# Performance work log

Hardware: AMD Instinct MI355X
Metric: run time of the kernel (lower is better)

The kernel has to match this reference:

```python
import jax, jax.numpy as jnp
import numpy as np

B, N, C, H = 2, 4096, 256, 4
EPS = 1e-12  # torch F.normalize eps


def setup_inputs() -> dict:
    key = jax.random.key(0)
    k1, k2, k3, k4 = jax.random.split(key, 4)
    x = jax.random.normal(k1, (B, N, C), dtype=jnp.float32)
    w_qkv = jax.random.normal(k2, (3 * C, C), dtype=jnp.float32) * (1.0 / np.sqrt(C))
    w_out = jax.random.normal(k3, (C, C), dtype=jnp.float32) * (1.0 / np.sqrt(C))
    b_out = jnp.zeros((C,), dtype=jnp.float32)
    temperature = jnp.ones((H, 1, 1), dtype=jnp.float32)
    return {"x": x, "w_qkv": w_qkv, "w_out": w_out, "b_out": b_out,
            "temperature": temperature}


def _l2norm(t):
    # torch.nn.functional.normalize(t, dim=-1): t / max(||t||_2, eps)
    n = jnp.sqrt(jnp.sum(t * t, axis=-1, keepdims=True))
    return t / jnp.maximum(n, EPS)


def reference(x, w_qkv, w_out, b_out, temperature):
    b, n, c = x.shape
    d = c // H
    qkv = x @ w_qkv.T                                   # [B,N,3C]
    qkv = qkv.reshape(b, n, 3, H, d).transpose(2, 0, 3, 1, 4)  # [3,B,H,N,d]
    q, k, v = qkv[0], qkv[1], qkv[2]                    # each [B,H,N,d]
    # transpose(-2,-1) -> [B,H,d,N]; normalize along N (per channel over tokens)
    q = _l2norm(jnp.swapaxes(q, -2, -1))                # [B,H,d,N]
    k = _l2norm(jnp.swapaxes(k, -2, -1))                # [B,H,d,N]
    v = jnp.swapaxes(v, -2, -1)                         # [B,H,d,N]
    # attn[n,m] = sum_d q[d,n] * k[d,m], scaled by learned per-head temperature
    attn = jnp.einsum('bhdn,bhdm->bhnm', q, k) * temperature  # [B,H,N,N]
    attn = jax.nn.softmax(attn, axis=-1)
    # (attn @ v^T): [B,H,N,N] @ [B,H,N,d] -> [B,H,N,d]
    out = jnp.einsum('bhnm,bhdm->bhnd', attn, v)        # [B,H,N,d]
    # faithful to source: permute(0,3,1,2) -> [B,d,H,N], then reshape(B,N,C)
    out = out.transpose(0, 3, 1, 2).reshape(b, n, c)
    return out @ w_out.T + b_out
```

## Files before the change

### kernel.cpp

```cpp
#include <hip/hip_runtime.h>

typedef _Float16 f16;
typedef f16 f16x8 __attribute__((ext_vector_type(8)));
typedef f16 f16x4 __attribute__((ext_vector_type(4)));
typedef __fp16 fp16x2 __attribute__((ext_vector_type(2)));
typedef float f32x4 __attribute__((ext_vector_type(4)));
typedef float f32x16 __attribute__((ext_vector_type(16)));
typedef unsigned int u32;

#define NTOK 4096

#define GLL(gsrc, ldst) \
  __builtin_amdgcn_global_load_lds( \
      (const __attribute__((address_space(1))) void*)(gsrc), \
      (__attribute__((address_space(3))) void*)(ldst), 16, 0, 0)

__global__ __launch_bounds__(256) void k_cvt(
    const float* __restrict__ x, const float* __restrict__ wq,
    const float* __restrict__ wo,
    f16* __restrict__ xb, f16* __restrict__ wqb, f16* __restrict__ wob)
{
  const int bx = blockIdx.x;
  const float* src; f16* dst; int off;
  if (bx < 2048)      { src = x;  dst = xb;  off = bx * 1024; }
  else if (bx < 2240) { src = wq; dst = wqb; off = (bx - 2048) * 1024; }
  else                { src = wo; dst = wob; off = (bx - 2240) * 1024; }
  const int i = off + threadIdx.x * 4;
  float4 f = *(const float4*)(src + i);
  f16x4 h;
  h[0] = (f16)f.x; h[1] = (f16)f.y; h[2] = (f16)f.z; h[3] = (f16)f.w;
  *(f16x4*)(dst + i) = h;
}

__global__ __launch_bounds__(256) void k_gemm(
    const f16* __restrict__ A, const f16* __restrict__ W,
    int K, int mode,
    f16* __restrict__ Qb, f16* __restrict__ Kb, f16* __restrict__ Vtb,
    float* __restrict__ outF, const float* __restrict__ bias,
    float* __restrict__ partQ, float* __restrict__ partK)
{
  __shared__ f16 Al[64 * 40];
  __shared__ f16 Wl[64 * 40];
  __shared__ float redl[4][64];
  const int t = threadIdx.x;
  const int w = t >> 6, l = t & 63;
  const int lrow = l & 15, lk = l >> 4;
  const int m0 = blockIdx.y * 64, nc0 = blockIdx.x * 64;
  f32x4 acc[4] = {};
  const int srow = t >> 2, sseg = t & 3;
  for (int k0 = 0; k0 < K; k0 += 32) {
    __syncthreads();
    f16x8 av = *(const f16x8*)(A + (size_t)(m0 + srow) * K + k0 + sseg * 8);
    f16x8 wv = *(const f16x8*)(W + (size_t)(nc0 + srow) * K + k0 + sseg * 8);
    *(f16x8*)(Al + srow * 40 + sseg * 8) = av;
    *(f16x8*)(Wl + srow * 40 + sseg * 8) = wv;
    __syncthreads();
    f16x8 af = *(const f16x8*)(Al + (w * 16 + lrow) * 40 + lk * 8);
#pragma unroll
    for (int ct = 0; ct < 4; ++ct) {
      f16x8 bf = *(const f16x8*)(Wl + (ct * 16 + lrow) * 40 + lk * 8);
      acc[ct] = __builtin_amdgcn_mfma_f32_16x16x32_f16(af, bf, acc[ct], 0, 0, 0);
    }
  }
  const int nb = m0 + w * 16 + lk * 4;
  if (mode == 0) {
    const int b = nb >> 12, n = nb & 4095;
#pragma unroll
    for (int ct = 0; ct < 4; ++ct) {
      int gc = nc0 + ct * 16 + lrow;
      int s = gc >> 8, h = (gc >> 6) & 3, dd = gc & 63;
      int bh = b * 4 + h;
      if (s == 2) {
        f16x4 v;
#pragma unroll
        for (int j = 0; j < 4; ++j) v[j] = (f16)acc[ct][j];
        *(f16x4*)(Vtb + ((size_t)bh * 64 + dd) * 4096 + n) = v;
      } else {
        f16* dst = (s == 0) ? Qb : Kb;
#pragma unroll
        for (int j = 0; j < 4; ++j)
          dst[((size_t)bh * 4096 + n + j) * 64 + dd] = (f16)acc[ct][j];
      }
    }
    if (nc0 < 512) {
#pragma unroll
      for (int ct = 0; ct < 4; ++ct) {
        float v = acc[ct][0] * acc[ct][0] + acc[ct][1] * acc[ct][1]
                + acc[ct][2] * acc[ct][2] + acc[ct][3] * acc[ct][3];
        v += __shfl_xor(v, 16, 64);
        v += __shfl_xor(v, 32, 64);
        if (lk == 0) redl[w][ct * 16 + lrow] = v;
      }
      __syncthreads();
      if (t < 64) {
        float sq = redl[0][t] + redl[1][t] + redl[2][t] + redl[3][t];
        const int s = nc0 >> 8, h2 = (nc0 >> 6) & 3;
        const int b2 = m0 >> 12, mb = (m0 >> 6) & 63;
        float* dst = (s == 0) ? partQ : partK;
        dst[((b2 * 4 + h2) * 64 + mb) * 64 + t] = sq;
      }
    }
  } else {
#pragma unroll
    for (int ct = 0; ct < 4; ++ct) {
      int gc = nc0 + ct * 16 + lrow;
      float bv = bias[gc];
#pragma unroll
      for (int j = 0; j < 4; ++j)
        outF[(size_t)(nb + j) * 256 + gc] = acc[ct][j] + bv;
    }
  }
}

__global__ __launch_bounds__(512) void k_norm2(
    const float* __restrict__ partQ, const float* __restrict__ partK,
    const float* __restrict__ temp, f16* __restrict__ cqh)
{
  const int t = threadIdx.x;
  const int bh = t >> 6, dd = t & 63;
  float sq = 0.f, sk = 0.f;
  for (int s = 0; s < 64; ++s) {
    sq += partQ[(bh * 64 + s) * 64 + dd];
    sk += partK[(bh * 64 + s) * 64 + dd];
  }
  float c = temp[bh & 3] * 1.4426950408889634f /
            (fmaxf(sqrtf(sq), 1e-12f) * fmaxf(sqrtf(sk), 1e-12f));
  cqh[t] = (f16)c;
}

__device__ inline void plane_swap(u32& a, u32& b) {
  asm volatile("v_permlane32_swap_b32 %0, %1" : "+v"(a), "+v"(b));
}

__global__ __launch_bounds__(512, 2) void k_flash5(
    const f16* __restrict__ Qb, const f16* __restrict__ Kb,
    const f16* __restrict__ Vtb, const f16* __restrict__ cqh,
    f16* __restrict__ Y)
{
  __shared__ f16 KVl[32768];
  __shared__ float Lsh[512];
  const int t = threadIdx.x, w = t >> 6, l = t & 63;
  const int r = l & 31, hi = l >> 5;
  const int ks = w >> 1, qh = w & 1;
  const int r7 = r & 7;
  int nb2 = (blockIdx.x & 7) * 32 + (blockIdx.x >> 3);
  const int bh = nb2 >> 5, qt = nb2 & 31;
  const size_t base = (size_t)bh * NTOK * 64;
  f16x8 qf[2][4];
  {
    const f16* cp = cqh + bh * 64;
#pragma unroll
    for (int s = 0; s < 2; ++s) {
      const f16* qp = Qb + base + (size_t)(qt * 128 + qh * 64 + s * 32 + r) * 64 + hi * 8;
#pragma unroll
      for (int c = 0; c < 4; ++c)
        qf[s][c] = *(const f16x8*)(qp + c * 16) * *(const f16x8*)(cp + c * 16 + hi * 8);
    }
  }
  const f16* srcK = Kb + base + (size_t)(w * 8 + (l >> 3)) * 64 + ((l & 7) ^ (l >> 3)) * 8;
  const int vrow = w * 4 + (l >> 4);
  const f16* srcV = Vtb + base + (size_t)vrow * 4096 + ((l & 15) ^ (vrow & 7)) * 8;
  const int dK = w * 8 * 64;
  const int dV = 8192 + w * 4 * 128;
#define STAGE(cur, tile) { \
    const f16* sk_ = srcK + (size_t)(tile) * 8192; \
    const f16* sv_ = srcV + (tile) * 128; \
    GLL(sk_,          KVl + (cur) * 16384 + dK); \
    GLL(sk_ + 4096,   KVl + (cur) * 16384 + dK + 4096); \
    GLL(sv_,          KVl + (cur) * 16384 + dV); \
    GLL(sv_ + 131072, KVl + (cur) * 16384 + dV + 4096); }
  const int kro = (ks * 32 + r) * 64;
  const int kc0 = ((0 + hi) ^ r7) * 8, kc1 = ((2 + hi) ^ r7) * 8;
  const int kc2 = ((4 + hi) ^ r7) * 8, kc3 = ((6 + hi) ^ r7) * 8;
  const int vb0 = 8192 + r * 128, vb1 = 8192 + (32 + r) * 128;
  const int vc0 = ((ks * 4 + 0 + hi) ^ r7) * 8, vc1 = ((ks * 4 + 2 + hi) ^ r7) * 8;

#define QKSTEP(SACC, QS) { \
    SACC = (f32x16){}; \
    SACC = __builtin_amdgcn_mfma_f32_32x32x16_f16(kf0, qf[QS][0], SACC, 0, 0, 0); \
    SACC = __builtin_amdgcn_mfma_f32_32x32x16_f16(kf1, qf[QS][1], SACC, 0, 0, 0); \
    SACC = __builtin_amdgcn_mfma_f32_32x32x16_f16(kf2, qf[QS][2], SACC, 0, 0, 0); \
    SACC = __builtin_amdgcn_mfma_f32_32x32x16_f16(kf3, qf[QS][3], SACC, 0, 0, 0); }

#define SMPV(SACC, LS, OIDX, V0, V1, V2, V3) { \
    u32 Dw[8]; \
    _Pragma("unroll") \
    for (int u = 0; u < 4; ++u) { \
      _Pragma("unroll") \
      for (int v = 0; v < 2; ++v) { \
        float a  = exp2f(SACC[u * 4 + v * 2]); \
        float b2 = exp2f(SACC[u * 4 + v * 2 + 1]); \
        LS += a + b2; \
        union { fp16x2 h; u32 u; } cv; \
        cv.h = __builtin_amdgcn_cvt_pkrtz(a, b2); \
        Dw[u * 2 + v] = cv.u; \
      } \
    } \
    plane_swap(Dw[0], Dw[2]); \
    plane_swap(Dw[1], Dw[3]); \
    plane_swap(Dw[4], Dw[6]); \
    plane_swap(Dw[5], Dw[7]); \
    union { f16x8 v; u32 d[4]; } p0, p1; \
    p0.d[0] = Dw[0]; p0.d[1] = Dw[1]; p0.d[2] = Dw[2]; p0.d[3] = Dw[3]; \
    p1.d[0] = Dw[4]; p1.d[1] = Dw[5]; p1.d[2] = Dw[6]; p1.d[3] = Dw[7]; \
    __builtin_amdgcn_s_setprio(1); \
    oacc[OIDX][0] = __builtin_amdgcn_mfma_f32_32x32x16_f16(p0.v, V0, oacc[OIDX][0], 0, 0, 0); \
    oacc[OIDX][0] = __builtin_amdgcn_mfma_f32_32x32x16_f16(p1.v, V1, oacc[OIDX][0], 0, 0, 0); \
    oacc[OIDX][1] = __builtin_amdgcn_mfma_f32_32x32x16_f16(p0.v, V2, oacc[OIDX][1], 0, 0, 0); \
    oacc[OIDX][1] = __builtin_amdgcn_mfma_f32_32x32x16_f16(p1.v, V3, oacc[OIDX][1], 0, 0, 0); \
    __builtin_amdgcn_s_setprio(0); }

  f32x16 oacc[2][2] = {};
  f32x16 saccA = {}, saccB = {};
  float ls0 = 0.f, ls1 = 0.f;
  f16x8 vfp0 = {}, vfp1 = {}, vfp2 = {}, vfp3 = {};
  STAGE(0, 0);
  __syncthreads();
  for (int tl = 0; tl < 32; ++tl) {
    const int cur = tl & 1;
    const f16* Bb = KVl + cur * 16384;
    f16x8 kf0 = *(const f16x8*)(Bb + kro + kc0);
    f16x8 kf1 = *(const f16x8*)(Bb + kro + kc1);
    f16x8 kf2 = *(const f16x8*)(Bb + kro + kc2);
    f16x8 kf3 = *(const f16x8*)(Bb + kro + kc3);
    f16x8 vfc0 = *(const f16x8*)(Bb + vb0 + vc0);
    f16x8 vfc1 = *(const f16x8*)(Bb + vb0 + vc1);
    f16x8 vfc2 = *(const f16x8*)(Bb + vb1 + vc0);
    f16x8 vfc3 = *(const f16x8*)(Bb + vb1 + vc1);
    if (tl < 31) STAGE(cur ^ 1, tl + 1);
    __builtin_amdgcn_s_setprio(1);
    QKSTEP(saccA, 0);
    __builtin_amdgcn_s_setprio(0);
    if (tl > 0) SMPV(saccB, ls1, 1, vfp0, vfp1, vfp2, vfp3);
    __builtin_amdgcn_s_setprio(1);
    QKSTEP(saccB, 1);
    __builtin_amdgcn_s_setprio(0);
    SMPV(saccA, ls0, 0, vfc0, vfc1, vfc2, vfc3);
    vfp0 = vfc0; vfp1 = vfc1; vfp2 = vfc2; vfp3 = vfc3;
    __syncthreads();
  }
  SMPV(saccB, ls1, 1, vfp0, vfp1, vfp2, vfp3);
#undef STAGE
#undef QKSTEP
#undef SMPV
  ls0 += __shfl_xor(ls0, 32, 64);
  ls1 += __shfl_xor(ls1, 32, 64);
  if (hi == 0) { Lsh[w * 64 + r] = ls0; Lsh[w * 64 + 32 + r] = ls1; }
#pragma unroll
  for (int s = 0; s < 2; ++s)
#pragma unroll
    for (int dt = 0; dt < 2; ++dt) {
      f16* orow = KVl + w * 4096 + (dt * 32 + r) * 64;
      const f32x16& oa = oacc[s][dt];
#pragma unroll
      for (int u = 0; u < 4; ++u) {
        f16x4 h4;
        h4[0] = (f16)oa[u * 4 + 0]; h4[1] = (f16)oa[u * 4 + 1];
        h4[2] = (f16)oa[u * 4 + 2]; h4[3] = (f16)oa[u * 4 + 3];
        *(f16x4*)(orow + (((s * 4 + u) ^ r7) * 8) + hi * 4) = h4;
      }
    }
  __syncthreads();
  const int s2 = w >> 2, dt2 = (w >> 1) & 1, qh2 = w & 1;
  const int b = bh >> 2, h = bh & 3;
#pragma unroll
  for (int c = 0; c < 2; ++c) {
    float accv[8] = {}, denv[8] = {};
#pragma unroll
    for (int ksl = 0; ksl < 4; ++ksl) {
      const int wp = ksl * 2 + qh2;
      f16x8 rd = *(const f16x8*)(KVl + wp * 4096 + (dt2 * 32 + r) * 64 +
                                 (((s2 * 4 + hi * 2 + c) ^ r7) * 8));
      f32x4 la = *(const f32x4*)(Lsh + wp * 64 + s2 * 32 + hi * 16 + c * 8);
      f32x4 lb = *(const f32x4*)(Lsh + wp * 64 + s2 * 32 + hi * 16 + c * 8 + 4);
#pragma unroll
      for (int j = 0; j < 4; ++j) {
        accv[j]     += (float)rd[j];
        accv[4 + j] += (float)rd[4 + j];
        denv[j]     += la[j];
        denv[4 + j] += lb[j];
      }
    }
    const int ng = qt * 128 + qh2 * 64 + s2 * 32 + hi * 16 + c * 8;
    const int np = (dt2 * 32 + r) * 64 + h * 16 + (ng >> 8);
    const int cp_ = ng & 255;
    f16x8 yv;
#pragma unroll
    for (int j = 0; j < 8; ++j) yv[j] = (f16)(accv[j] / denv[j]);
    *(f16x8*)(Y + ((size_t)b * 4096 + np) * 256 + cp_) = yv;
  }
}

extern "C" void kernel_launch(void* const* d_in, const int* in_sizes, int n_in,
                              void* d_out, int out_size, void* d_ws, size_t ws_size,
                              hipStream_t stream)
{
  const float* x     = (const float*)d_in[0];
  const float* w_qkv = (const float*)d_in[1];
  const float* w_out = (const float*)d_in[2];
  const float* b_out = (const float*)d_in[3];
  const float* temp  = (const float*)d_in[4];

  char* ws = (char*)d_ws;
  f16*   xb    = (f16*)(ws);
  f16*   wqkvb = (f16*)(ws + 4 * 1024 * 1024);
  f16*   woutb = (f16*)(ws + 4 * 1024 * 1024 + 512 * 1024);
  f16*   Qb    = (f16*)(ws + 5  * 1024 * 1024);
  f16*   Kb    = (f16*)(ws + 9  * 1024 * 1024);
  f16*   Vtb   = (f16*)(ws + 13 * 1024 * 1024);
  f16*   cqh   = (f16*)(ws + 17 * 1024 * 1024);
  float* partQ = (float*)(ws + 17 * 1024 * 1024 + 8192);
  float* partK = (float*)(ws + 17 * 1024 * 1024 + 8192 + 131072);
  f16*   Y     = (f16*)(ws + 18 * 1024 * 1024);
  float* outF  = (float*)d_out;

  k_cvt<<<2304, 256, 0, stream>>>(x, w_qkv, w_out, xb, wqkvb, woutb);
  k_gemm<<<dim3(12, 128), 256, 0, stream>>>(xb, wqkvb, 256, 0, Qb, Kb, Vtb,
                                            nullptr, nullptr, partQ, partK);
  k_norm2<<<1, 512, 0, stream>>>(partQ, partK, temp, cqh);
  k_flash5<<<256, 512, 0, stream>>>(Qb, Kb, Vtb, cqh, Y);
  k_gemm<<<dim3(4, 128), 256, 0, stream>>>(Y, woutb, 256, 1, nullptr, nullptr, nullptr,
                                           outF, b_out, nullptr, nullptr);
}
```

Measured before the change: 88.59 us.

## Split attention over two KV halves with a combine kernel

The flash kernel now splits each query tile's key range into two halves. The grid doubles from 256 to 512 blocks, and launch bounds are raised to 4 blocks per CU to fill more CUs. Each half writes an unnormalized fp16 partial output and row sums, and a new combine kernel adds them and divides. The software pipelining of QK and softmax·V across iterations is removed, and exp2 now uses the hardware builtin. This trades an extra launch and extra global traffic for partials, plus reduced intra-wave overlap, for better occupancy. Workspace buffers are aliased to reuse dead regions.

```diff
diff --git a/kernel.cpp b/kernel.cpp
--- a/kernel.cpp
+++ b/kernel.cpp
@@ -132,10 +132,11 @@
   asm volatile("v_permlane32_swap_b32 %0, %1" : "+v"(a), "+v"(b));
 }
 
-__global__ __launch_bounds__(512, 2) void k_flash5(
+__global__ __launch_bounds__(512, 4) void k_flash7(
     const f16* __restrict__ Qb, const f16* __restrict__ Kb,
     const f16* __restrict__ Vtb, const f16* __restrict__ cqh,
-    f16* __restrict__ Y)
+    f16* __restrict__ Opart0, f16* __restrict__ Opart1,
+    float* __restrict__ Lsum0, float* __restrict__ Lsum1)
 {
   __shared__ f16 KVl[32768];
   __shared__ float Lsh[512];
@@ -143,8 +144,12 @@
   const int r = l & 31, hi = l >> 5;
   const int ks = w >> 1, qh = w & 1;
   const int r7 = r & 7;
-  int nb2 = (blockIdx.x & 7) * 32 + (blockIdx.x >> 3);
-  const int bh = nb2 >> 5, qt = nb2 & 31;
+  int nb2 = (blockIdx.x & 7) * 64 + (blockIdx.x >> 3);
+  const int bh = nb2 >> 6, rest = nb2 & 63;
+  const int qt = rest >> 1, kv = rest & 1;
+  const int koff = kv * 2048;
+  f16* Opart = kv ? Opart1 : Opart0;
+  float* Lsum = kv ? Lsum1 : Lsum0;
   const size_t base = (size_t)bh * NTOK * 64;
   f16x8 qf[2][4];
   {
@@ -157,11 +162,11 @@
         qf[s][c] = *(const f16x8*)(qp + c * 16) * *(const f16x8*)(cp + c * 16 + hi * 8);
     }
   }
-  const f16* srcK = Kb + base + (size_t)(w * 8 + (l >> 3)) * 64 + ((l & 7) ^ (l >> 3)) * 8;
+  const f16* srcK = Kb + base + (size_t)(koff + w * 8 + (l >> 3)) * 64 + ((l & 7) ^ (l >> 3)) * 8;
   const int vrow = w * 4 + (l >> 4);
-  const f16* srcV = Vtb + base + (size_t)vrow * 4096 + ((l & 15) ^ (vrow & 7)) * 8;
-  const int dK = w * 8 * 64;
-  const int dV = 8192 + w * 4 * 128;
+  const f16* srcV = Vtb + base + (size_t)vrow * 4096 + koff + ((l & 15) ^ (vrow & 7)) * 8;
+  const int dK = w * 512;
+  const int dV = 8192 + w * 512;
 #define STAGE(cur, tile) { \
     const f16* sk_ = srcK + (size_t)(tile) * 8192; \
     const f16* sv_ = srcV + (tile) * 128; \
@@ -175,22 +180,22 @@
   const int vb0 = 8192 + r * 128, vb1 = 8192 + (32 + r) * 128;
   const int vc0 = ((ks * 4 + 0 + hi) ^ r7) * 8, vc1 = ((ks * 4 + 2 + hi) ^ r7) * 8;
 
-#define QKSTEP(SACC, QS) { \
-    SACC = (f32x16){}; \
-    SACC = __builtin_amdgcn_mfma_f32_32x32x16_f16(kf0, qf[QS][0], SACC, 0, 0, 0); \
-    SACC = __builtin_amdgcn_mfma_f32_32x32x16_f16(kf1, qf[QS][1], SACC, 0, 0, 0); \
-    SACC = __builtin_amdgcn_mfma_f32_32x32x16_f16(kf2, qf[QS][2], SACC, 0, 0, 0); \
-    SACC = __builtin_amdgcn_mfma_f32_32x32x16_f16(kf3, qf[QS][3], SACC, 0, 0, 0); }
-
-#define SMPV(SACC, LS, OIDX, V0, V1, V2, V3) { \
+#define SET_STEP(S, LSVAR) { \
+    f32x16 sacc = {}; \
+    __builtin_amdgcn_s_setprio(1); \
+    sacc = __builtin_amdgcn_mfma_f32_32x32x16_f16(kf0, qf[S][0], sacc, 0, 0, 0); \
+    sacc = __builtin_amdgcn_mfma_f32_32x32x16_f16(kf1, qf[S][1], sacc, 0, 0, 0); \
+    sacc = __builtin_amdgcn_mfma_f32_32x32x16_f16(kf2, qf[S][2], sacc, 0, 0, 0); \
+    sacc = __builtin_amdgcn_mfma_f32_32x32x16_f16(kf3, qf[S][3], sacc, 0, 0, 0); \
+    __builtin_amdgcn_s_setprio(0); \
     u32 Dw[8]; \
     _Pragma("unroll") \
     for (int u = 0; u < 4; ++u) { \
       _Pragma("unroll") \
       for (int v = 0; v < 2; ++v) { \
-        float a  = exp2f(SACC[u * 4 + v * 2]); \
-        float b2 = exp2f(SACC[u * 4 + v * 2 + 1]); \
-        LS += a + b2; \
+        float a  = __builtin_amdgcn_exp2f(sacc[u * 4 + v * 2]); \
+        float b2 = __builtin_amdgcn_exp2f(sacc[u * 4 + v * 2 + 1]); \
+        LSVAR += a + b2; \
         union { fp16x2 h; u32 u; } cv; \
         cv.h = __builtin_amdgcn_cvt_pkrtz(a, b2); \
         Dw[u * 2 + v] = cv.u; \
@@ -204,45 +209,34 @@
     p0.d[0] = Dw[0]; p0.d[1] = Dw[1]; p0.d[2] = Dw[2]; p0.d[3] = Dw[3]; \
     p1.d[0] = Dw[4]; p1.d[1] = Dw[5]; p1.d[2] = Dw[6]; p1.d[3] = Dw[7]; \
     __builtin_amdgcn_s_setprio(1); \
-    oacc[OIDX][0] = __builtin_amdgcn_mfma_f32_32x32x16_f16(p0.v, V0, oacc[OIDX][0], 0, 0, 0); \
-    oacc[OIDX][0] = __builtin_amdgcn_mfma_f32_32x32x16_f16(p1.v, V1, oacc[OIDX][0], 0, 0, 0); \
-    oacc[OIDX][1] = __builtin_amdgcn_mfma_f32_32x32x16_f16(p0.v, V2, oacc[OIDX][1], 0, 0, 0); \
-    oacc[OIDX][1] = __builtin_amdgcn_mfma_f32_32x32x16_f16(p1.v, V3, oacc[OIDX][1], 0, 0, 0); \
+    oacc[S][0] = __builtin_amdgcn_mfma_f32_32x32x16_f16(p0.v, vf0, oacc[S][0], 0, 0, 0); \
+    oacc[S][0] = __builtin_amdgcn_mfma_f32_32x32x16_f16(p1.v, vf1, oacc[S][0], 0, 0, 0); \
+    oacc[S][1] = __builtin_amdgcn_mfma_f32_32x32x16_f16(p0.v, vf2, oacc[S][1], 0, 0, 0); \
+    oacc[S][1] = __builtin_amdgcn_mfma_f32_32x32x16_f16(p1.v, vf3, oacc[S][1], 0, 0, 0); \
     __builtin_amdgcn_s_setprio(0); }
 
   f32x16 oacc[2][2] = {};
-  f32x16 saccA = {}, saccB = {};
   float ls0 = 0.f, ls1 = 0.f;
-  f16x8 vfp0 = {}, vfp1 = {}, vfp2 = {}, vfp3 = {};
   STAGE(0, 0);
   __syncthreads();
-  for (int tl = 0; tl < 32; ++tl) {
+  for (int tl = 0; tl < 16; ++tl) {
     const int cur = tl & 1;
     const f16* Bb = KVl + cur * 16384;
     f16x8 kf0 = *(const f16x8*)(Bb + kro + kc0);
     f16x8 kf1 = *(const f16x8*)(Bb + kro + kc1);
     f16x8 kf2 = *(const f16x8*)(Bb + kro + kc2);
     f16x8 kf3 = *(const f16x8*)(Bb + kro + kc3);
-    f16x8 vfc0 = *(const f16x8*)(Bb + vb0 + vc0);
-    f16x8 vfc1 = *(const f16x8*)(Bb + vb0 + vc1);
-    f16x8 vfc2 = *(const f16x8*)(Bb + vb1 + vc0);
-    f16x8 vfc3 = *(const f16x8*)(Bb + vb1 + vc1);
-    if (tl < 31) STAGE(cur ^ 1, tl + 1);
-    __builtin_amdgcn_s_setprio(1);
-    QKSTEP(saccA, 0);
-    __builtin_amdgcn_s_setprio(0);
-    if (tl > 0) SMPV(saccB, ls1, 1, vfp0, vfp1, vfp2, vfp3);
-    __builtin_amdgcn_s_setprio(1);
-    QKSTEP(saccB, 1);
-    __builtin_amdgcn_s_setprio(0);
-    SMPV(saccA, ls0, 0, vfc0, vfc1, vfc2, vfc3);
-    vfp0 = vfc0; vfp1 = vfc1; vfp2 = vfc2; vfp3 = vfc3;
+    f16x8 vf0 = *(const f16x8*)(Bb + vb0 + vc0);
+    f16x8 vf1 = *(const f16x8*)(Bb + vb0 + vc1);
+    f16x8 vf2 = *(const f16x8*)(Bb + vb1 + vc0);
+    f16x8 vf3 = *(const f16x8*)(Bb + vb1 + vc1);
+    if (tl < 15) STAGE(cur ^ 1, tl + 1);
+    SET_STEP(0, ls0);
+    SET_STEP(1, ls1);
     __syncthreads();
   }
-  SMPV(saccB, ls1, 1, vfp0, vfp1, vfp2, vfp3);
 #undef STAGE
-#undef QKSTEP
-#undef SMPV
+#undef SET_STEP
   ls0 += __shfl_xor(ls0, 32, 64);
   ls1 += __shfl_xor(ls1, 32, 64);
   if (hi == 0) { Lsh[w * 64 + r] = ls0; Lsh[w * 64 + 32 + r] = ls1; }
@@ -262,7 +256,7 @@
     }
   __syncthreads();
   const int s2 = w >> 2, dt2 = (w >> 1) & 1, qh2 = w & 1;
-  const int b = bh >> 2, h = bh & 3;
+  const int blk = bh * 32 + qt;
 #pragma unroll
   for (int c = 0; c < 2; ++c) {
     float accv[8] = {}, denv[8] = {};
@@ -281,13 +275,51 @@
         denv[4 + j] += lb[j];
       }
     }
-    const int ng = qt * 128 + qh2 * 64 + s2 * 32 + hi * 16 + c * 8;
-    const int np = (dt2 * 32 + r) * 64 + h * 16 + (ng >> 8);
-    const int cp_ = ng & 255;
+    const int dd = dt2 * 32 + r;
+    const int qloc = qh2 * 64 + (s2 * 4 + hi * 2 + c) * 8;
+    f16x8 ov;
+#pragma unroll
+    for (int j = 0; j < 8; ++j) ov[j] = (f16)accv[j];
+    *(f16x8*)(Opart + (size_t)blk * 8192 + dd * 128 + qloc) = ov;
+    if (dt2 == 0) {
+      f32x4 d0, d1;
+      d0[0] = denv[0]; d0[1] = denv[1]; d0[2] = denv[2]; d0[3] = denv[3];
+      d1[0] = denv[4]; d1[1] = denv[5]; d1[2] = denv[6]; d1[3] = denv[7];
+      *(f32x4*)(Lsum + blk * 128 + qloc) = d0;
+      *(f32x4*)(Lsum + blk * 128 + qloc + 4) = d1;
+    }
+  }
+}
+
+__global__ __launch_bounds__(256) void k_comb(
+    const f16* __restrict__ Opart0, const f16* __restrict__ Opart1,
+    const float* __restrict__ Lsum0, const float* __restrict__ Lsum1,
+    f16* __restrict__ Y)
+{
+  const int blk = blockIdx.x;
+  const int bh = blk >> 5, qt = blk & 31;
+  const int b = bh >> 2, h = bh & 3;
+  const int t = threadIdx.x;
+  const int dd = t >> 2, qc = t & 3;
+#pragma unroll
+  for (int j = 0; j < 4; ++j) {
+    const int ql = qc * 32 + j * 8;
+    f16x8 A = *(const f16x8*)(Opart0 + (size_t)blk * 8192 + dd * 128 + ql);
+    f16x8 Bv = *(const f16x8*)(Opart1 + (size_t)blk * 8192 + dd * 128 + ql);
+    f32x4 la0 = *(const f32x4*)(Lsum0 + blk * 128 + ql);
+    f32x4 la1 = *(const f32x4*)(Lsum0 + blk * 128 + ql + 4);
+    f32x4 lb0 = *(const f32x4*)(Lsum1 + blk * 128 + ql);
+    f32x4 lb1 = *(const f32x4*)(Lsum1 + blk * 128 + ql + 4);
+    const int ng = qt * 128 + ql;
+    const int np = dd * 64 + h * 16 + (ng >> 8);
+    const int cp = ng & 255;
     f16x8 yv;
 #pragma unroll
-    for (int j = 0; j < 8; ++j) yv[j] = (f16)(accv[j] / denv[j]);
-    *(f16x8*)(Y + ((size_t)b * 4096 + np) * 256 + cp_) = yv;
+    for (int jj = 0; jj < 4; ++jj) {
+      yv[jj]     = (f16)(((float)A[jj]     + (float)Bv[jj])     / (la0[jj] + lb0[jj]));
+      yv[4 + jj] = (f16)(((float)A[4 + jj] + (float)Bv[4 + jj]) / (la1[jj] + lb1[jj]));
+    }
+    *(f16x8*)(Y + ((size_t)b * 4096 + np) * 256 + cp) = yv;
   }
 }
 
@@ -302,23 +334,28 @@
   const float* temp  = (const float*)d_in[4];
 
   char* ws = (char*)d_ws;
-  f16*   xb    = (f16*)(ws);
-  f16*   wqkvb = (f16*)(ws + 4 * 1024 * 1024);
-  f16*   woutb = (f16*)(ws + 4 * 1024 * 1024 + 512 * 1024);
-  f16*   Qb    = (f16*)(ws + 5  * 1024 * 1024);
-  f16*   Kb    = (f16*)(ws + 9  * 1024 * 1024);
-  f16*   Vtb   = (f16*)(ws + 13 * 1024 * 1024);
-  f16*   cqh   = (f16*)(ws + 17 * 1024 * 1024);
-  float* partQ = (float*)(ws + 17 * 1024 * 1024 + 8192);
-  float* partK = (float*)(ws + 17 * 1024 * 1024 + 8192 + 131072);
-  f16*   Y     = (f16*)(ws + 18 * 1024 * 1024);
-  float* outF  = (float*)d_out;
+  f16*   xb     = (f16*)(ws);
+  f16*   Opart0 = (f16*)(ws);
+  f16*   wqkvb  = (f16*)(ws + 4 * 1024 * 1024);
+  float* Lsum0  = (float*)(ws + 4 * 1024 * 1024);
+  float* Lsum1  = (float*)(ws + 4 * 1024 * 1024 + 131072);
+  f16*   Qb     = (f16*)(ws + 5  * 1024 * 1024);
+  f16*   Y      = (f16*)(ws + 5  * 1024 * 1024);
+  f16*   Kb     = (f16*)(ws + 9  * 1024 * 1024);
+  f16*   Vtb    = (f16*)(ws + 13 * 1024 * 1024);
+  f16*   cqh    = (f16*)(ws + 17 * 1024 * 1024);
+  float* partQ  = (float*)(ws + 17 * 1024 * 1024 + 8192);
+  float* partK  = (float*)(ws + 17 * 1024 * 1024 + 8192 + 131072);
+  f16*   woutb  = (f16*)(ws + 17 * 1024 * 1024 + 512 * 1024);
+  f16*   Opart1 = (f16*)(ws + 18 * 1024 * 1024);
+  float* outF   = (float*)d_out;
 
   k_cvt<<<2304, 256, 0, stream>>>(x, w_qkv, w_out, xb, wqkvb, woutb);
   k_gemm<<<dim3(12, 128), 256, 0, stream>>>(xb, wqkvb, 256, 0, Qb, Kb, Vtb,
                                             nullptr, nullptr, partQ, partK);
   k_norm2<<<1, 512, 0, stream>>>(partQ, partK, temp, cqh);
-  k_flash5<<<256, 512, 0, stream>>>(Qb, Kb, Vtb, cqh, Y);
+  k_flash7<<<512, 512, 0, stream>>>(Qb, Kb, Vtb, cqh, Opart0, Opart1, Lsum0, Lsum1);
+  k_comb<<<256, 256, 0, stream>>>(Opart0, Opart1, Lsum0, Lsum1, Y);
   k_gemm<<<dim3(4, 128), 256, 0, stream>>>(Y, woutb, 256, 1, nullptr, nullptr, nullptr,
                                            outF, b_out, nullptr, nullptr);
 }
```

Measured after the change: 340.1 us. 3.84x slower.
